# Optimization experiments

Measured on AMD Instinct MI355X. Metric: run time of the kernel, lower is better.

The kernel has to match this reference:

```python
import jax, jax.numpy as jnp
import numpy as np

VOCAB, EMB, HID, OUT = 50257, 256, 512, 2
SEQ, BATCH = 512, 64


def setup_inputs() -> dict:
    key = jax.random.key(0)
    ks = jax.random.split(key, 8)
    s_ih = 1.0 / np.sqrt(HID)
    return {
        "text": jax.random.randint(ks[0], (SEQ, BATCH), 0, VOCAB, dtype=jnp.int64)
            if jax.config.jax_enable_x64 else jax.random.randint(ks[0], (SEQ, BATCH), 0, VOCAB, dtype=jnp.int32),
        "emb_table": jax.random.normal(ks[1], (VOCAB, EMB), dtype=jnp.float32),
        "W_ih": jax.random.uniform(ks[2], (HID, EMB), jnp.float32, -s_ih, s_ih),
        "W_hh": jax.random.uniform(ks[3], (HID, HID), jnp.float32, -s_ih, s_ih),
        "b_ih": jax.random.uniform(ks[4], (HID,), jnp.float32, -s_ih, s_ih),
        "b_hh": jax.random.uniform(ks[5], (HID,), jnp.float32, -s_ih, s_ih),
        "W_fc": jax.random.uniform(ks[6], (OUT, HID), jnp.float32, -s_ih, s_ih),
        "b_fc": jax.random.uniform(ks[7], (OUT,), jnp.float32, -s_ih, s_ih),
    }


def reference(text, emb_table, W_ih, W_hh, b_ih, b_hh, W_fc, b_fc):
    # embedded: [seq, batch, emb]
    embedded = emb_table[text]
    h0 = jnp.zeros((text.shape[1], HID), dtype=emb_table.dtype)

    def step(h, x_t):
        # torch.nn.RNNCell (tanh): h' = tanh(x W_ih^T + b_ih + h W_hh^T + b_hh)
        h_new = jnp.tanh(x_t @ W_ih.T + b_ih + h @ W_hh.T + b_hh)
        return h_new, None

    h_final, _ = jax.lax.scan(step, h0, embedded)
    return h_final @ W_fc.T + b_fc
```

## Files before the change

kernel.cpp:

```cpp
#include <hip/hip_runtime.h>
#include <hip/hip_fp16.h>

#define SEQ   512
#define BATCH 64
#define EMB   256
#define HID   512

#define CR 192
#define CL 64
#define WLROW 68

typedef _Float16 half2v  __attribute__((ext_vector_type(2)));
typedef _Float16 half8v  __attribute__((ext_vector_type(8)));
typedef _Float16 half32v __attribute__((ext_vector_type(32)));

__device__ __forceinline__ float dot2acc(half2v a, half2v b, float c) {
#if defined(__has_builtin)
#if __has_builtin(__builtin_amdgcn_fdot2)
  return __builtin_amdgcn_fdot2(a, b, c, false);
#else
  return fmaf((float)a[0], (float)b[0], fmaf((float)a[1], (float)b[1], c));
#endif
#else
  return fmaf((float)a[0], (float)b[0], fmaf((float)a[1], (float)b[1], c));
#endif
}

__device__ __forceinline__ float fast_tanh(float x) {
  x = fminf(fmaxf(x, -15.f), 15.f);
  float e = __expf(2.f * x);
  return (e - 1.f) / (e + 1.f);
}

__device__ __forceinline__ half32v load32f(const float* p) {
  const float4* q = reinterpret_cast<const float4*>(p);
  float4 v0=q[0],v1=q[1],v2=q[2],v3=q[3],v4=q[4],v5=q[5],v6=q[6],v7=q[7];
  half32v r = {
    (_Float16)v0.x,(_Float16)v0.y,(_Float16)v0.z,(_Float16)v0.w,
    (_Float16)v1.x,(_Float16)v1.y,(_Float16)v1.z,(_Float16)v1.w,
    (_Float16)v2.x,(_Float16)v2.y,(_Float16)v2.z,(_Float16)v2.w,
    (_Float16)v3.x,(_Float16)v3.y,(_Float16)v3.z,(_Float16)v3.w,
    (_Float16)v4.x,(_Float16)v4.y,(_Float16)v4.z,(_Float16)v4.w,
    (_Float16)v5.x,(_Float16)v5.y,(_Float16)v5.z,(_Float16)v5.w,
    (_Float16)v6.x,(_Float16)v6.y,(_Float16)v6.z,(_Float16)v6.w,
    (_Float16)v7.x,(_Float16)v7.y,(_Float16)v7.z,(_Float16)v7.w };
  return r;
}

template<int M>
__device__ __forceinline__ void dot4(half32v wv, half8v hv,
                                     float& a0, float& a1, float& a2, float& a3) {
  a0 = dot2acc(__builtin_shufflevector(wv, wv, 8*M+0, 8*M+1),
               __builtin_shufflevector(hv, hv, 0, 1), a0);
  a1 = dot2acc(__builtin_shufflevector(wv, wv, 8*M+2, 8*M+3),
               __builtin_shufflevector(hv, hv, 2, 3), a1);
  a2 = dot2acc(__builtin_shufflevector(wv, wv, 8*M+4, 8*M+5),
               __builtin_shufflevector(hv, hv, 4, 5), a2);
  a3 = dot2acc(__builtin_shufflevector(wv, wv, 8*M+6, 8*M+7),
               __builtin_shufflevector(hv, hv, 6, 7), a3);
}

__device__ __forceinline__ void dot_chunk(half32v wv, const half8v* hp, int qb,
                                          float& a0, float& a1, float& a2, float& a3) {
  dot4<0>(wv, hp[qb + 0], a0, a1, a2, a3);
  dot4<1>(wv, hp[qb + 1], a0, a1, a2, a3);
  dot4<2>(wv, hp[qb + 2], a0, a1, a2, a3);
  dot4<3>(wv, hp[qb + 3], a0, a1, a2, a3);
}

__global__ __launch_bounds__(512) void proj_kernel(
    const int* __restrict__ text, const float* __restrict__ emb,
    const float* __restrict__ Wih, const float* __restrict__ bih,
    const float* __restrict__ bhh, __half* __restrict__ X) {
  __shared__ __align__(16) __half se[BATCH][EMB];
  __shared__ int stok[BATCH];

  const int t = blockIdx.x;
  const int j = threadIdx.x;

  if (j < BATCH) stok[j] = text[t * BATCH + j];
  __syncthreads();

  {
    const int r = j >> 3;
    const int c0 = (j & 7) * 32;
    const float4* src = reinterpret_cast<const float4*>(emb + (size_t)stok[r] * EMB + c0);
    half2v* rowp = reinterpret_cast<half2v*>(&se[r][0]);
#pragma unroll
    for (int q = 0; q < 8; ++q) {
      float4 v = src[q];
      half2v p0; p0[0] = (_Float16)v.x; p0[1] = (_Float16)v.y;
      half2v p1; p1[0] = (_Float16)v.z; p1[1] = (_Float16)v.w;
      rowp[c0 / 2 + 2 * q + 0] = p0;
      rowp[c0 / 2 + 2 * q + 1] = p1;
    }
  }
  __syncthreads();

  float acc[BATCH];
#pragma unroll
  for (int b = 0; b < BATCH; ++b) acc[b] = 0.f;

  for (int ec = 0; ec < EMB / 32; ++ec) {
    half2v wh[16];
    const float4* wp = reinterpret_cast<const float4*>(Wih + (size_t)j * EMB + ec * 32);
#pragma unroll
    for (int q = 0; q < 8; ++q) {
      float4 v = wp[q];
      wh[2 * q + 0][0] = (_Float16)v.x; wh[2 * q + 0][1] = (_Float16)v.y;
      wh[2 * q + 1][0] = (_Float16)v.z; wh[2 * q + 1][1] = (_Float16)v.w;
    }
#pragma unroll
    for (int b = 0; b < BATCH; ++b) {
      const half8v* ep = reinterpret_cast<const half8v*>(&se[b][ec * 32]);
      float a = acc[b];
#pragma unroll
      for (int r = 0; r < 4; ++r) {
        half8v ev = ep[r];
        a = dot2acc(wh[4*r+0], __builtin_shufflevector(ev, ev, 0, 1), a);
        a = dot2acc(wh[4*r+1], __builtin_shufflevector(ev, ev, 2, 3), a);
        a = dot2acc(wh[4*r+2], __builtin_shufflevector(ev, ev, 4, 5), a);
        a = dot2acc(wh[4*r+3], __builtin_shufflevector(ev, ev, 6, 7), a);
      }
      acc[b] = a;
    }
  }

  const float bias = bih[j] + bhh[j];
#pragma unroll
  for (int b = 0; b < BATCH; ++b)
    X[((size_t)t * BATCH + b) * HID + j] = __float2half(acc[b] + bias);
}

__global__
__attribute__((amdgpu_flat_work_group_size(512, 512), amdgpu_waves_per_eu(2, 2)))
void rnn_kernel(
    const __half* __restrict__ X, const float* __restrict__ Whh,
    const float* __restrict__ Wfc, const float* __restrict__ bfc,
    float* __restrict__ out) {
  __shared__ __align__(16) half2v Wl[HID * WLROW];
  __shared__ __align__(16) half2v h2[2][HID / 2];
  __shared__ float red[16];

  const int j = threadIdx.x;
  const int b = blockIdx.x;

  const float* wr = Whh + (size_t)j * HID;

  half32v w0  = load32f(wr +   0), w1  = load32f(wr +  32), w2  = load32f(wr +  64);
  half32v w3  = load32f(wr +  96), w4  = load32f(wr + 128), w5  = load32f(wr + 160);
  half32v w6  = load32f(wr + 192), w7  = load32f(wr + 224), w8  = load32f(wr + 256);
  half32v w9  = load32f(wr + 288), w10 = load32f(wr + 320), w11 = load32f(wr + 352);

#pragma unroll
  for (int c = 0; c < CL; ++c) {
    float2 v = reinterpret_cast<const float2*>(wr)[CR + c];
    half2v hh; hh[0] = (_Float16)v.x; hh[1] = (_Float16)v.y;
    Wl[j * WLROW + c] = hh;
  }
  if (j < HID / 2) {
    half2v z; z[0] = (_Float16)0.f; z[1] = (_Float16)0.f;
    h2[0][j] = z;
  }
  __syncthreads();

  const __half* Xp = X + (size_t)b * HID + j;
  float xv = __half2float(Xp[0]);
  float h = 0.f;
  int cur = 0;

  for (int t = 0; t < SEQ; ++t) {
    const int tn = (t < SEQ - 1) ? t + 1 : t;
    float xnext = __half2float(Xp[(size_t)tn * BATCH * HID]);

    const half8v* hp = reinterpret_cast<const half8v*>(&h2[cur][0]);
    const half8v* wl = reinterpret_cast<const half8v*>(&Wl[j * WLROW]);

    float a0 = 0.f, a1 = 0.f, a2 = 0.f, a3 = 0.f;
    dot_chunk(w0,  hp,  0, a0, a1, a2, a3);
    dot_chunk(w1,  hp,  4, a0, a1, a2, a3);
    dot_chunk(w2,  hp,  8, a0, a1, a2, a3);
    dot_chunk(w3,  hp, 12, a0, a1, a2, a3);
    dot_chunk(w4,  hp, 16, a0, a1, a2, a3);
    dot_chunk(w5,  hp, 20, a0, a1, a2, a3);
    dot_chunk(w6,  hp, 24, a0, a1, a2, a3);
    dot_chunk(w7,  hp, 28, a0, a1, a2, a3);
    dot_chunk(w8,  hp, 32, a0, a1, a2, a3);
    dot_chunk(w9,  hp, 36, a0, a1, a2, a3);
    dot_chunk(w10, hp, 40, a0, a1, a2, a3);
    dot_chunk(w11, hp, 44, a0, a1, a2, a3);

#pragma unroll
    for (int q = 0; q < CL / 4; ++q) {
      half8v hv = hp[CR / 4 + q];
      half8v wv = wl[q];
      a0 = dot2acc(__builtin_shufflevector(wv, wv, 0, 1),
                   __builtin_shufflevector(hv, hv, 0, 1), a0);
      a1 = dot2acc(__builtin_shufflevector(wv, wv, 2, 3),
                   __builtin_shufflevector(hv, hv, 2, 3), a1);
      a2 = dot2acc(__builtin_shufflevector(wv, wv, 4, 5),
                   __builtin_shufflevector(hv, hv, 4, 5), a2);
      a3 = dot2acc(__builtin_shufflevector(wv, wv, 6, 7),
                   __builtin_shufflevector(hv, hv, 6, 7), a3);
    }

    float acc = ((a0 + a1) + (a2 + a3)) + xv;
    h = fast_tanh(acc);
    xv = xnext;

    reinterpret_cast<__half*>(&h2[cur ^ 1][0])[j] = __float2half(h);
    __syncthreads();
    cur ^= 1;
  }

  float c0 = Wfc[j] * h;
  float c1 = Wfc[HID + j] * h;
#pragma unroll
  for (int o = 32; o > 0; o >>= 1) {
    c0 += __shfl_down(c0, o, 64);
    c1 += __shfl_down(c1, o, 64);
  }
  const int wave = j >> 6;
  if ((j & 63) == 0) { red[wave] = c0; red[8 + wave] = c1; }
  __syncthreads();
  if (j == 0) {
    float s0 = 0.f, s1 = 0.f;
#pragma unroll
    for (int i = 0; i < 8; ++i) { s0 += red[i]; s1 += red[8 + i]; }
    out[b * 2 + 0] = s0 + bfc[0];
    out[b * 2 + 1] = s1 + bfc[1];
  }
}

extern "C" void kernel_launch(void* const* d_in, const int* in_sizes, int n_in,
                              void* d_out, int out_size, void* d_ws, size_t ws_size,
                              hipStream_t stream) {
  const int*   text = (const int*)d_in[0];
  const float* emb  = (const float*)d_in[1];
  const float* Wih  = (const float*)d_in[2];
  const float* Whh  = (const float*)d_in[3];
  const float* bih  = (const float*)d_in[4];
  const float* bhh  = (const float*)d_in[5];
  const float* Wfc  = (const float*)d_in[6];
  const float* bfc  = (const float*)d_in[7];
  float* outp = (float*)d_out;

  __half* X = (__half*)d_ws;

  proj_kernel<<<SEQ, 512, 0, stream>>>(text, emb, Wih, bih, bhh, X);
  rnn_kernel<<<BATCH, 512, 0, stream>>>(X, Whh, Wfc, bfc, outp);
}
```

Measured before the change: 999.2 us.

## Split each hidden row's recurrent dot product across two threads

The RNN kernel now launches 1024 threads per block, with two threads per hidden unit. Each thread holds half of the register-resident W_hh row (6 chunks instead of 12) and half of the LDS-resident tail, and the two partial sums are combined with a lane shuffle. The aim is to halve the serial dot-product latency of each timestep and to relieve register pressure. The cost is a wider block barrier every step, an extra shuffle, and half the threads sitting idle on the h write.

```diff
diff --git a/kernel.cpp b/kernel.cpp
--- a/kernel.cpp
+++ b/kernel.cpp
@@ -6,9 +6,10 @@
 #define EMB   256
 #define HID   512
 
-#define CR 192
-#define CL 64
+#define RC 96
+#define LCT 32
 #define WLROW 68
+#define SL1 36
 
 typedef _Float16 half2v  __attribute__((ext_vector_type(2)));
 typedef _Float16 half8v  __attribute__((ext_vector_type(8)));
@@ -132,67 +133,72 @@
     X[((size_t)t * BATCH + b) * HID + j] = __float2half(acc[b] + bias);
 }
 
-__global__
-__attribute__((amdgpu_flat_work_group_size(512, 512), amdgpu_waves_per_eu(2, 2)))
-void rnn_kernel(
+__global__ __launch_bounds__(1024) void rnn_kernel(
     const __half* __restrict__ X, const float* __restrict__ Whh,
     const float* __restrict__ Wfc, const float* __restrict__ bfc,
     float* __restrict__ out) {
   __shared__ __align__(16) half2v Wl[HID * WLROW];
   __shared__ __align__(16) half2v h2[2][HID / 2];
-  __shared__ float red[16];
-
-  const int j = threadIdx.x;
-  const int b = blockIdx.x;
-
-  const float* wr = Whh + (size_t)j * HID;
-
-  half32v w0  = load32f(wr +   0), w1  = load32f(wr +  32), w2  = load32f(wr +  64);
-  half32v w3  = load32f(wr +  96), w4  = load32f(wr + 128), w5  = load32f(wr + 160);
-  half32v w6  = load32f(wr + 192), w7  = load32f(wr + 224), w8  = load32f(wr + 256);
-  half32v w9  = load32f(wr + 288), w10 = load32f(wr + 320), w11 = load32f(wr + 352);
-
-#pragma unroll
-  for (int c = 0; c < CL; ++c) {
-    float2 v = reinterpret_cast<const float2*>(wr)[CR + c];
-    half2v hh; hh[0] = (_Float16)v.x; hh[1] = (_Float16)v.y;
-    Wl[j * WLROW + c] = hh;
-  }
-  if (j < HID / 2) {
+  __shared__ float red[32];
+
+  const int tid = threadIdx.x;
+  const int r   = tid >> 1;
+  const int hf  = tid & 1;
+  const int b   = blockIdx.x;
+
+  const float* wr = Whh + (size_t)r * HID;
+
+  {
+    const int dst0 = r * WLROW + (hf ? SL1 : 0);
+#pragma unroll
+    for (int c = 0; c < LCT; ++c) {
+      float2 v = reinterpret_cast<const float2*>(wr)[192 + hf * LCT + c];
+      half2v hh; hh[0] = (_Float16)v.x; hh[1] = (_Float16)v.y;
+      Wl[dst0 + c] = hh;
+    }
+  }
+  if (tid < HID / 2) {
     half2v z; z[0] = (_Float16)0.f; z[1] = (_Float16)0.f;
-    h2[0][j] = z;
-  }
-  __syncthreads();
-
-  const __half* Xp = X + (size_t)b * HID + j;
+    h2[0][tid] = z;
+  }
+  __builtin_amdgcn_sched_barrier(0);
+
+  const float* wb = wr + hf * 192;
+  half32v w0 = load32f(wb +   0); __builtin_amdgcn_sched_barrier(0);
+  half32v w1 = load32f(wb +  32); __builtin_amdgcn_sched_barrier(0);
+  half32v w2 = load32f(wb +  64); __builtin_amdgcn_sched_barrier(0);
+  half32v w3 = load32f(wb +  96); __builtin_amdgcn_sched_barrier(0);
+  half32v w4 = load32f(wb + 128); __builtin_amdgcn_sched_barrier(0);
+  half32v w5 = load32f(wb + 160); __builtin_amdgcn_sched_barrier(0);
+
+  __syncthreads();
+
+  const __half* Xp = X + (size_t)b * HID + r;
   float xv = __half2float(Xp[0]);
   float h = 0.f;
   int cur = 0;
 
+  const int hq0 = hf * 24;
+  const int hq1 = 48 + hf * 8;
+  const half8v* wl = reinterpret_cast<const half8v*>(&Wl[r * WLROW + (hf ? SL1 : 0)]);
+
   for (int t = 0; t < SEQ; ++t) {
     const int tn = (t < SEQ - 1) ? t + 1 : t;
     float xnext = __half2float(Xp[(size_t)tn * BATCH * HID]);
 
     const half8v* hp = reinterpret_cast<const half8v*>(&h2[cur][0]);
-    const half8v* wl = reinterpret_cast<const half8v*>(&Wl[j * WLROW]);
 
     float a0 = 0.f, a1 = 0.f, a2 = 0.f, a3 = 0.f;
-    dot_chunk(w0,  hp,  0, a0, a1, a2, a3);
-    dot_chunk(w1,  hp,  4, a0, a1, a2, a3);
-    dot_chunk(w2,  hp,  8, a0, a1, a2, a3);
-    dot_chunk(w3,  hp, 12, a0, a1, a2, a3);
-    dot_chunk(w4,  hp, 16, a0, a1, a2, a3);
-    dot_chunk(w5,  hp, 20, a0, a1, a2, a3);
-    dot_chunk(w6,  hp, 24, a0, a1, a2, a3);
-    dot_chunk(w7,  hp, 28, a0, a1, a2, a3);
-    dot_chunk(w8,  hp, 32, a0, a1, a2, a3);
-    dot_chunk(w9,  hp, 36, a0, a1, a2, a3);
-    dot_chunk(w10, hp, 40, a0, a1, a2, a3);
-    dot_chunk(w11, hp, 44, a0, a1, a2, a3);
-
-#pragma unroll
-    for (int q = 0; q < CL / 4; ++q) {
-      half8v hv = hp[CR / 4 + q];
+    dot_chunk(w0, hp, hq0 +  0, a0, a1, a2, a3);
+    dot_chunk(w1, hp, hq0 +  4, a0, a1, a2, a3);
+    dot_chunk(w2, hp, hq0 +  8, a0, a1, a2, a3);
+    dot_chunk(w3, hp, hq0 + 12, a0, a1, a2, a3);
+    dot_chunk(w4, hp, hq0 + 16, a0, a1, a2, a3);
+    dot_chunk(w5, hp, hq0 + 20, a0, a1, a2, a3);
+
+#pragma unroll
+    for (int q = 0; q < 8; ++q) {
+      half8v hv = hp[hq1 + q];
       half8v wv = wl[q];
       a0 = dot2acc(__builtin_shufflevector(wv, wv, 0, 1),
                    __builtin_shufflevector(hv, hv, 0, 1), a0);
@@ -204,29 +210,30 @@
                    __builtin_shufflevector(hv, hv, 6, 7), a3);
     }
 
-    float acc = ((a0 + a1) + (a2 + a3)) + xv;
-    h = fast_tanh(acc);
+    float part = ((a0 + a1) + (a2 + a3));
+    part += __shfl_xor(part, 1, 64);
+    h = fast_tanh(part + xv);
     xv = xnext;
 
-    reinterpret_cast<__half*>(&h2[cur ^ 1][0])[j] = __float2half(h);
+    if (hf == 0) reinterpret_cast<__half*>(&h2[cur ^ 1][0])[r] = __float2half(h);
     __syncthreads();
     cur ^= 1;
   }
 
-  float c0 = Wfc[j] * h;
-  float c1 = Wfc[HID + j] * h;
+  float c0 = hf ? 0.f : Wfc[r] * h;
+  float c1 = hf ? 0.f : Wfc[HID + r] * h;
 #pragma unroll
   for (int o = 32; o > 0; o >>= 1) {
     c0 += __shfl_down(c0, o, 64);
     c1 += __shfl_down(c1, o, 64);
   }
-  const int wave = j >> 6;
-  if ((j & 63) == 0) { red[wave] = c0; red[8 + wave] = c1; }
-  __syncthreads();
-  if (j == 0) {
+  const int wave = tid >> 6;
+  if ((tid & 63) == 0) { red[wave] = c0; red[16 + wave] = c1; }
+  __syncthreads();
+  if (tid == 0) {
     float s0 = 0.f, s1 = 0.f;
 #pragma unroll
-    for (int i = 0; i < 8; ++i) { s0 += red[i]; s1 += red[8 + i]; }
+    for (int i = 0; i < 16; ++i) { s0 += red[i]; s1 += red[16 + i]; }
     out[b * 2 + 0] = s0 + bfc[0];
     out[b * 2 + 1] = s1 + bfc[1];
   }
@@ -248,5 +255,5 @@
   __half* X = (__half*)d_ws;
 
   proj_kernel<<<SEQ, 512, 0, stream>>>(text, emb, Wih, bih, bhh, X);
-  rnn_kernel<<<BATCH, 512, 0, stream>>>(X, Whh, Wfc, bfc, outp);
-}
+  rnn_kernel<<<BATCH, 1024, 0, stream>>>(X, Whh, Wfc, bfc, outp);
+}
```

Result: slower. 1.138 ms (+13.9%).
